# Kernel optimization log

Hardware: AMD Instinct MI355X
Metric: run time of the kernel (lower is better)

Reference implementation:

```python
import jax, jax.numpy as jnp
import numpy as np

B, S, H = 64, 2048, 256
H3 = 3 * H


def setup_inputs() -> dict:
    key = jax.random.key(0)
    ks = jax.random.split(key, 5)
    static = jax.random.normal(ks[0], (B, S, H), dtype=jnp.float32)
    dynamic = jax.random.normal(ks[1], (B, S, H), dtype=jnp.float32)
    decoder_hidden = jax.random.normal(ks[2], (B, H), dtype=jnp.float32)
    # learned params (nn.Parameter in original); scale ~ 1/sqrt(fan_in)
    v = jax.random.normal(ks[3], (1, H3), dtype=jnp.float32) / np.sqrt(H3)
    W = jax.random.normal(ks[4], (H3, H3), dtype=jnp.float32) / np.sqrt(H3)
    return {"static": static, "dynamic": dynamic,
            "decoder_hidden": decoder_hidden, "v": v, "W": W}


def reference(static, dynamic, decoder_hidden, v, W):
    # cat = concat(static[i,j], dynamic[i,j], decoder_hidden[i]) -> [B, S, 3H]
    dec = jnp.broadcast_to(decoder_hidden[:, None, :], static.shape)
    cat = jnp.concatenate([static, dynamic, dec], axis=-1)
    # score[b,s] = v . tanh(W @ cat[b,s])
    hidden = jnp.tanh(jnp.einsum('ok,bsk->bso', W, cat))  # [B, S, 3H]
    scores = jnp.einsum('bso,o->bs', hidden, v[0])        # [B, S]
    return jax.nn.softmax(scores, axis=1)
```

## Files before the change

### kernel.cpp

```cpp
#include <hip/hip_runtime.h>
#include <hip/hip_bf16.h>

#define B_   64
#define S_   2048
#define H_   256
#define H3_  768
#define K_   512
#define MT   64
#define RSTR 1040

typedef __attribute__((ext_vector_type(8))) short  bf16x8;
typedef __attribute__((ext_vector_type(4))) float  f32x4;

__device__ __forceinline__ uint pkbf2(float a, float b) {
    float2 f = make_float2(a, b);
    __hip_bfloat162 h = __float22bfloat162_rn(f);
    return *reinterpret_cast<uint*>(&h);
}

__global__ void pack_w(const float* __restrict__ W, short* __restrict__ wpk) {
    int t = blockIdx.x * 256 + threadIdx.x;
    if (t >= 48 * 16 * 64) return;
    int lane = t & 63;
    int ks   = (t >> 6) & 15;
    int ot   = t >> 10;
    int o  = ot * 16 + (lane & 15);
    int kb = ks * 32 + (lane >> 4) * 8;
    const float* src = W + (size_t)o * H3_ + kb;
    float4 a = ((const float4*)src)[0];
    float4 b = ((const float4*)src)[1];
    uint4 pk;
    pk.x = pkbf2(a.x, a.y);
    pk.y = pkbf2(a.z, a.w);
    pk.z = pkbf2(b.x, b.y);
    pk.w = pkbf2(b.z, b.w);
    *(uint4*)(wpk + (size_t)t * 8) = pk;
}

__global__ void bias_k(const float* __restrict__ W, const float* __restrict__ dec,
                       const float* __restrict__ v, float* __restrict__ bias,
                       float* __restrict__ vsum) {
    if (blockIdx.x == 192) {
        if (threadIdx.x < 64) {
            float s = 0.f;
#pragma unroll
            for (int i = 0; i < 12; ++i) s += v[threadIdx.x + i * 64];
#pragma unroll
            for (int off = 32; off >= 1; off >>= 1) s += __shfl_xor(s, off);
            if (threadIdx.x == 0) vsum[0] = s;
        }
        return;
    }
    int idx = blockIdx.x * 256 + threadIdx.x;
    int b = idx / H3_;
    int o = idx - b * H3_;
    const float4* wr = (const float4*)(W + (size_t)o * H3_ + 2 * H_);
    const float4* dv = (const float4*)(dec + (size_t)b * H_);
    float s = 0.f;
#pragma unroll 8
    for (int k = 0; k < H_ / 4; ++k) {
        float4 a = wr[k], d = dv[k];
        s += a.x * d.x + a.y * d.y + a.z * d.z + a.w * d.w;
    }
    bias[idx] = s;
}

__global__ __launch_bounds__(256, 2)
void score_k(const float* __restrict__ stat, const float* __restrict__ dyn,
             const short* __restrict__ wpk, const float* __restrict__ bias,
             const float* __restrict__ v, const float* __restrict__ vsum,
             float* __restrict__ scores) {
    __shared__ char  aT[MT * RSTR];
    __shared__ float sred[4][MT];

    const int tid  = threadIdx.x;
    const int pos0 = blockIdx.x * MT;
    const int bidx = pos0 >> 11;

#pragma unroll
    for (int bat = 0; bat < 2; ++bat) {
        float4 f0[8], f1[8];
#pragma unroll
        for (int u = 0; u < 8; ++u) {
            int lin = (bat * 8 + u) * 256 + tid;
            int row = lin >> 6;
            int k   = (lin & 63) * 8;
            const float* src = (k < 256)
                ? (stat + (size_t)(pos0 + row) * H_ + k)
                : (dyn  + (size_t)(pos0 + row) * H_ + (k - 256));
            f0[u] = ((const float4*)src)[0];
            f1[u] = ((const float4*)src)[1];
        }
#pragma unroll
        for (int u = 0; u < 8; ++u) {
            int lin = (bat * 8 + u) * 256 + tid;
            int row = lin >> 6;
            int ux  = lin & 63;
            uint4 pk;
            pk.x = pkbf2(f0[u].x, f0[u].y);
            pk.y = pkbf2(f0[u].z, f0[u].w);
            pk.z = pkbf2(f1[u].x, f1[u].y);
            pk.w = pkbf2(f1[u].z, f1[u].w);
            *(uint4*)(aT + row * RSTR + ux * 16) = pk;
        }
    }
    __syncthreads();

    const int wave = tid >> 6;
    const int lane = tid & 63;
    const int lr = lane & 15;
    const int lg = lane >> 4;

    const char* abase = aT + lr * RSTR + lg * 16;

    float sacc[4][4];
#pragma unroll
    for (int mi = 0; mi < 4; ++mi)
#pragma unroll
        for (int j = 0; j < 4; ++j) sacc[mi][j] = 0.f;

    const float C1 = 2.8853900817779268f;

#pragma unroll 1
    for (int pass = 0; pass < 3; ++pass) {
        const int obase = pass * 256 + wave * 64;

        float bv[4], vv2[4];
#pragma unroll
        for (int ni = 0; ni < 4; ++ni) {
            int o = obase + ni * 16 + lr;
            bv[ni]  = bias[bidx * H3_ + o];
            vv2[ni] = -2.0f * v[o];
        }

        f32x4 acc[4][4];
#pragma unroll
        for (int mi = 0; mi < 4; ++mi)
#pragma unroll
            for (int ni = 0; ni < 4; ++ni) {
                f32x4 a = {bv[ni], bv[ni], bv[ni], bv[ni]};
                acc[mi][ni] = a;
            }

        const short* wp0 = wpk + ((size_t)((pass * 16 + wave * 4) * 16) * 64 + lane) * 8;

#pragma unroll 4
        for (int ks = 0; ks < 16; ++ks) {
            bf16x8 bfr[4];
#pragma unroll
            for (int ni = 0; ni < 4; ++ni)
                bfr[ni] = *(const bf16x8*)(wp0 + ni * 16 * 64 * 8 + ks * 64 * 8);
            bf16x8 afr[4];
#pragma unroll
            for (int mi = 0; mi < 4; ++mi)
                afr[mi] = *(const bf16x8*)(abase + mi * 16 * RSTR + ks * 64);
#pragma unroll
            for (int mi = 0; mi < 4; ++mi)
#pragma unroll
                for (int ni = 0; ni < 4; ++ni)
                    acc[mi][ni] = __builtin_amdgcn_mfma_f32_16x16x32_bf16(
                        afr[mi], bfr[ni], acc[mi][ni], 0, 0, 0);
        }

#pragma unroll
        for (int ni = 0; ni < 4; ++ni)
#pragma unroll
            for (int mi = 0; mi < 4; ++mi)
#pragma unroll
                for (int j = 0; j < 4; ++j) {
                    float e = __builtin_amdgcn_exp2f(acc[mi][ni][j] * C1);
                    float r = __builtin_amdgcn_rcpf(e + 1.0f);
                    sacc[mi][j] = fmaf(vv2[ni], r, sacc[mi][j]);
                }
    }

#pragma unroll
    for (int mi = 0; mi < 4; ++mi)
#pragma unroll
        for (int j = 0; j < 4; ++j) {
            float x = sacc[mi][j];
            x += __shfl_xor(x, 1);
            x += __shfl_xor(x, 2);
            x += __shfl_xor(x, 4);
            x += __shfl_xor(x, 8);
            sacc[mi][j] = x;
        }
    if (lr == 0) {
#pragma unroll
        for (int mi = 0; mi < 4; ++mi)
#pragma unroll
            for (int j = 0; j < 4; ++j)
                sred[wave][mi * 16 + lg * 4 + j] = sacc[mi][j];
    }
    __syncthreads();
    if (tid < MT) {
        float s = vsum[0] + sred[0][tid] + sred[1][tid] + sred[2][tid] + sred[3][tid];
        scores[pos0 + tid] = s;
    }
}

__global__ void softmax_k(float* __restrict__ out) {
    const int b = blockIdx.x;
    float* row = out + (size_t)b * S_;
    const int tid  = threadIdx.x;
    const int wave = tid >> 6;
    const int lane = tid & 63;

    float vals[8];
    float m = -1e30f;
#pragma unroll
    for (int i = 0; i < 8; ++i) {
        vals[i] = row[tid + i * 256];
        m = fmaxf(m, vals[i]);
    }
#pragma unroll
    for (int off = 32; off >= 1; off >>= 1) m = fmaxf(m, __shfl_xor(m, off));
    __shared__ float redm[4];
    __shared__ float reds[4];
    if (lane == 0) redm[wave] = m;
    __syncthreads();
    m = fmaxf(fmaxf(redm[0], redm[1]), fmaxf(redm[2], redm[3]));

    float s = 0.f;
#pragma unroll
    for (int i = 0; i < 8; ++i) {
        vals[i] = __expf(vals[i] - m);
        s += vals[i];
    }
#pragma unroll
    for (int off = 32; off >= 1; off >>= 1) s += __shfl_xor(s, off);
    if (lane == 0) reds[wave] = s;
    __syncthreads();
    s = reds[0] + reds[1] + reds[2] + reds[3];
    float inv = 1.0f / s;
#pragma unroll
    for (int i = 0; i < 8; ++i) row[tid + i * 256] = vals[i] * inv;
}

extern "C" void kernel_launch(void* const* d_in, const int* in_sizes, int n_in,
                              void* d_out, int out_size, void* d_ws, size_t ws_size,
                              hipStream_t stream) {
    const float* stat = (const float*)d_in[0];
    const float* dyn  = (const float*)d_in[1];
    const float* dec  = (const float*)d_in[2];
    const float* v    = (const float*)d_in[3];
    const float* W    = (const float*)d_in[4];
    float* out = (float*)d_out;

    short* wpk  = (short*)d_ws;
    float* bias = (float*)((char*)d_ws + (size_t)H3_ * K_ * 2);
    float* vsum = bias + B_ * H3_;

    pack_w <<<(48 * 16 * 64 + 255) / 256, 256, 0, stream>>>(W, wpk);
    bias_k <<<193, 256, 0, stream>>>(W, dec, v, bias, vsum);
    score_k<<<(B_ * S_) / MT, 256, 0, stream>>>(stat, dyn, wpk, bias, v, vsum, out);
    softmax_k<<<B_, 256, 0, stream>>>(out);
}
```

Baseline: 147.7 us.

## Make score kernel persistent with double-buffered LDS prefetch across row tiles

The score kernel now launches 256 blocks of 512 threads. Each block processes 8 consecutive 64-row tiles, using double-buffered LDS. Global loads of the next tile's static and dynamic rows are interleaved between the MFMA phases of the current tile, so memory latency overlaps compute. Each of the 8 waves now owns 96 output columns, and bias and v are loaded once per block instead of per tile. This doubles LDS use and register pressure, and uses fewer, larger blocks, which may leave occupancy or load balance uneven.

```diff
diff --git a/kernel.cpp b/kernel.cpp
--- a/kernel.cpp
+++ b/kernel.cpp
@@ -7,7 +7,10 @@
 #define H3_  768
 #define K_   512
 #define MT   64
+#define TPB  8
+#define NB   256
 #define RSTR 1040
+#define BUFB (MT * RSTR)
 
 typedef __attribute__((ext_vector_type(8))) short  bf16x8;
 typedef __attribute__((ext_vector_type(4))) float  f32x4;
@@ -65,137 +68,214 @@
     bias[idx] = s;
 }
 
-__global__ __launch_bounds__(256, 2)
+__global__ __launch_bounds__(512, 2)
 void score_k(const float* __restrict__ stat, const float* __restrict__ dyn,
              const short* __restrict__ wpk, const float* __restrict__ bias,
              const float* __restrict__ v, const float* __restrict__ vsum,
              float* __restrict__ scores) {
-    __shared__ char  aT[MT * RSTR];
-    __shared__ float sred[4][MT];
+    __shared__ char  aT[2 * BUFB];
+    __shared__ float sred[2][8][MT];
 
     const int tid  = threadIdx.x;
-    const int pos0 = blockIdx.x * MT;
-    const int bidx = pos0 >> 11;
-
-#pragma unroll
-    for (int bat = 0; bat < 2; ++bat) {
-        float4 f0[8], f1[8];
-#pragma unroll
-        for (int u = 0; u < 8; ++u) {
-            int lin = (bat * 8 + u) * 256 + tid;
-            int row = lin >> 6;
-            int k   = (lin & 63) * 8;
-            const float* src = (k < 256)
-                ? (stat + (size_t)(pos0 + row) * H_ + k)
-                : (dyn  + (size_t)(pos0 + row) * H_ + (k - 256));
-            f0[u] = ((const float4*)src)[0];
-            f1[u] = ((const float4*)src)[1];
-        }
-#pragma unroll
-        for (int u = 0; u < 8; ++u) {
-            int lin = (bat * 8 + u) * 256 + tid;
-            int row = lin >> 6;
-            int ux  = lin & 63;
-            uint4 pk;
-            pk.x = pkbf2(f0[u].x, f0[u].y);
-            pk.y = pkbf2(f0[u].z, f0[u].w);
-            pk.z = pkbf2(f1[u].x, f1[u].y);
-            pk.w = pkbf2(f1[u].z, f1[u].w);
-            *(uint4*)(aT + row * RSTR + ux * 16) = pk;
-        }
-    }
-    __syncthreads();
-
     const int wave = tid >> 6;
     const int lane = tid & 63;
-    const int lr = lane & 15;
-    const int lg = lane >> 4;
-
-    const char* abase = aT + lr * RSTR + lg * 16;
-
-    float sacc[4][4];
-#pragma unroll
-    for (int mi = 0; mi < 4; ++mi)
-#pragma unroll
-        for (int j = 0; j < 4; ++j) sacc[mi][j] = 0.f;
-
+    const int lr   = lane & 15;
+    const int lg   = lane >> 4;
+
+    const int row0 = blockIdx.x * (TPB * MT);
+    const int bidx = row0 >> 11;
+
+    const float vs = vsum[0];
+
+    float bvA[2][3], vvA[2][3];
+#pragma unroll
+    for (int p = 0; p < 2; ++p)
+#pragma unroll
+        for (int ni = 0; ni < 3; ++ni) {
+            int o = wave * 96 + p * 48 + ni * 16 + lr;
+            bvA[p][ni] = bias[bidx * H3_ + o];
+            vvA[p][ni] = -2.0f * v[o];
+        }
+
+    const int kcol = lane * 8;
+    const float* srcbase = (kcol < 256) ? (stat + kcol) : (dyn + (kcol - 256));
+
+    float4 f0[3], f1[3];
+    auto loadu = [&](int u0, int n, int grow0) {
+#pragma unroll
+        for (int i = 0; i < n; ++i) {
+            int row = (u0 + i) * 8 + wave;
+            const float4* p = (const float4*)(srcbase + (size_t)(grow0 + row) * H_);
+            f0[i] = p[0];
+            f1[i] = p[1];
+        }
+    };
+    auto writeu = [&](int u0, int n, int bufoff) {
+#pragma unroll
+        for (int i = 0; i < n; ++i) {
+            int row = (u0 + i) * 8 + wave;
+            uint4 pk;
+            pk.x = pkbf2(f0[i].x, f0[i].y);
+            pk.y = pkbf2(f0[i].z, f0[i].w);
+            pk.z = pkbf2(f1[i].x, f1[i].y);
+            pk.w = pkbf2(f1[i].z, f1[i].w);
+            *(uint4*)(aT + bufoff + row * RSTR + lane * 16) = pk;
+        }
+    };
+
+    loadu(0, 3, row0); writeu(0, 3, 0);
+    loadu(3, 3, row0); writeu(3, 3, 0);
+    loadu(6, 2, row0); writeu(6, 2, 0);
+    __syncthreads();
+
+    const char* abase0 = aT + lr * RSTR + lg * 16;
     const float C1 = 2.8853900817779268f;
 
 #pragma unroll 1
-    for (int pass = 0; pass < 3; ++pass) {
-        const int obase = pass * 256 + wave * 64;
-
-        float bv[4], vv2[4];
-#pragma unroll
-        for (int ni = 0; ni < 4; ++ni) {
-            int o = obase + ni * 16 + lr;
-            bv[ni]  = bias[bidx * H3_ + o];
-            vv2[ni] = -2.0f * v[o];
-        }
-
-        f32x4 acc[4][4];
+    for (int t = 0; t < TPB; ++t) {
+        const int pos0 = row0 + t * MT;
+        const int cbuf = (t & 1) * BUFB;
+        const int nbuf = ((t & 1) ^ 1) * BUFB;
+        const int grown = pos0 + MT;
+        const bool pre = (t < TPB - 1);
+        const char* abase = abase0 + cbuf;
+
+        float sacc[4][4];
 #pragma unroll
         for (int mi = 0; mi < 4; ++mi)
 #pragma unroll
-            for (int ni = 0; ni < 4; ++ni) {
-                f32x4 a = {bv[ni], bv[ni], bv[ni], bv[ni]};
-                acc[mi][ni] = a;
+            for (int j = 0; j < 4; ++j) sacc[mi][j] = 0.f;
+
+        if (pre) loadu(0, 3, grown);
+
+        {
+            f32x4 acc[4][3];
+#pragma unroll
+            for (int mi = 0; mi < 4; ++mi)
+#pragma unroll
+                for (int ni = 0; ni < 3; ++ni) {
+                    f32x4 a = {bvA[0][ni], bvA[0][ni], bvA[0][ni], bvA[0][ni]};
+                    acc[mi][ni] = a;
+                }
+            const short* wp0 = wpk + (size_t)(wave * 6) * 8192 + lane * 8;
+#pragma unroll 4
+            for (int ks = 0; ks < 16; ++ks) {
+                bf16x8 bfr[3];
+#pragma unroll
+                for (int ni = 0; ni < 3; ++ni)
+                    bfr[ni] = *(const bf16x8*)(wp0 + ni * 8192 + ks * 512);
+                bf16x8 afr[4];
+#pragma unroll
+                for (int mi = 0; mi < 4; ++mi)
+                    afr[mi] = *(const bf16x8*)(abase + mi * (16 * RSTR) + ks * 64);
+#pragma unroll
+                for (int mi = 0; mi < 4; ++mi)
+#pragma unroll
+                    for (int ni = 0; ni < 3; ++ni)
+                        acc[mi][ni] = __builtin_amdgcn_mfma_f32_16x16x32_bf16(
+                            afr[mi], bfr[ni], acc[mi][ni], 0, 0, 0);
             }
-
-        const short* wp0 = wpk + ((size_t)((pass * 16 + wave * 4) * 16) * 64 + lane) * 8;
-
+#pragma unroll
+            for (int ni = 0; ni < 3; ++ni)
+#pragma unroll
+                for (int mi = 0; mi < 4; ++mi)
+#pragma unroll
+                    for (int j = 0; j < 4; ++j) {
+                        float e = __builtin_amdgcn_exp2f(acc[mi][ni][j] * C1);
+                        float r = __builtin_amdgcn_rcpf(e + 1.0f);
+                        sacc[mi][j] = fmaf(vvA[0][ni], r, sacc[mi][j]);
+                    }
+        }
+
+        if (pre) { writeu(0, 3, nbuf); loadu(3, 3, grown); }
+
+        {
+            f32x4 acc[4][3];
+#pragma unroll
+            for (int mi = 0; mi < 4; ++mi)
+#pragma unroll
+                for (int ni = 0; ni < 3; ++ni) {
+                    f32x4 a = {bvA[1][ni], bvA[1][ni], bvA[1][ni], bvA[1][ni]};
+                    acc[mi][ni] = a;
+                }
+            const short* wp1 = wpk + (size_t)(wave * 6 + 3) * 8192 + lane * 8;
 #pragma unroll 4
-        for (int ks = 0; ks < 16; ++ks) {
-            bf16x8 bfr[4];
-#pragma unroll
-            for (int ni = 0; ni < 4; ++ni)
-                bfr[ni] = *(const bf16x8*)(wp0 + ni * 16 * 64 * 8 + ks * 64 * 8);
-            bf16x8 afr[4];
+            for (int ks = 0; ks < 8; ++ks) {
+                bf16x8 bfr[3];
+#pragma unroll
+                for (int ni = 0; ni < 3; ++ni)
+                    bfr[ni] = *(const bf16x8*)(wp1 + ni * 8192 + ks * 512);
+                bf16x8 afr[4];
+#pragma unroll
+                for (int mi = 0; mi < 4; ++mi)
+                    afr[mi] = *(const bf16x8*)(abase + mi * (16 * RSTR) + ks * 64);
+#pragma unroll
+                for (int mi = 0; mi < 4; ++mi)
+#pragma unroll
+                    for (int ni = 0; ni < 3; ++ni)
+                        acc[mi][ni] = __builtin_amdgcn_mfma_f32_16x16x32_bf16(
+                            afr[mi], bfr[ni], acc[mi][ni], 0, 0, 0);
+            }
+
+            if (pre) { writeu(3, 3, nbuf); loadu(6, 2, grown); }
+
+#pragma unroll 4
+            for (int ks = 8; ks < 16; ++ks) {
+                bf16x8 bfr[3];
+#pragma unroll
+                for (int ni = 0; ni < 3; ++ni)
+                    bfr[ni] = *(const bf16x8*)(wp1 + ni * 8192 + ks * 512);
+                bf16x8 afr[4];
+#pragma unroll
+                for (int mi = 0; mi < 4; ++mi)
+                    afr[mi] = *(const bf16x8*)(abase + mi * (16 * RSTR) + ks * 64);
+#pragma unroll
+                for (int mi = 0; mi < 4; ++mi)
+#pragma unroll
+                    for (int ni = 0; ni < 3; ++ni)
+                        acc[mi][ni] = __builtin_amdgcn_mfma_f32_16x16x32_bf16(
+                            afr[mi], bfr[ni], acc[mi][ni], 0, 0, 0);
+            }
+
+            if (pre) writeu(6, 2, nbuf);
+
+#pragma unroll
+            for (int ni = 0; ni < 3; ++ni)
+#pragma unroll
+                for (int mi = 0; mi < 4; ++mi)
+#pragma unroll
+                    for (int j = 0; j < 4; ++j) {
+                        float e = __builtin_amdgcn_exp2f(acc[mi][ni][j] * C1);
+                        float r = __builtin_amdgcn_rcpf(e + 1.0f);
+                        sacc[mi][j] = fmaf(vvA[1][ni], r, sacc[mi][j]);
+                    }
+        }
+
+#pragma unroll
+        for (int mi = 0; mi < 4; ++mi)
+#pragma unroll
+            for (int j = 0; j < 4; ++j) {
+                float x = sacc[mi][j];
+                x += __shfl_xor(x, 1);
+                x += __shfl_xor(x, 2);
+                x += __shfl_xor(x, 4);
+                x += __shfl_xor(x, 8);
+                sacc[mi][j] = x;
+            }
+        if (lr == 0) {
 #pragma unroll
             for (int mi = 0; mi < 4; ++mi)
-                afr[mi] = *(const bf16x8*)(abase + mi * 16 * RSTR + ks * 64);
-#pragma unroll
-            for (int mi = 0; mi < 4; ++mi)
-#pragma unroll
-                for (int ni = 0; ni < 4; ++ni)
-                    acc[mi][ni] = __builtin_amdgcn_mfma_f32_16x16x32_bf16(
-                        afr[mi], bfr[ni], acc[mi][ni], 0, 0, 0);
-        }
-
-#pragma unroll
-        for (int ni = 0; ni < 4; ++ni)
-#pragma unroll
-            for (int mi = 0; mi < 4; ++mi)
-#pragma unroll
-                for (int j = 0; j < 4; ++j) {
-                    float e = __builtin_amdgcn_exp2f(acc[mi][ni][j] * C1);
-                    float r = __builtin_amdgcn_rcpf(e + 1.0f);
-                    sacc[mi][j] = fmaf(vv2[ni], r, sacc[mi][j]);
-                }
-    }
-
-#pragma unroll
-    for (int mi = 0; mi < 4; ++mi)
-#pragma unroll
-        for (int j = 0; j < 4; ++j) {
-            float x = sacc[mi][j];
-            x += __shfl_xor(x, 1);
-            x += __shfl_xor(x, 2);
-            x += __shfl_xor(x, 4);
-            x += __shfl_xor(x, 8);
-            sacc[mi][j] = x;
-        }
-    if (lr == 0) {
-#pragma unroll
-        for (int mi = 0; mi < 4; ++mi)
-#pragma unroll
-            for (int j = 0; j < 4; ++j)
-                sred[wave][mi * 16 + lg * 4 + j] = sacc[mi][j];
-    }
-    __syncthreads();
-    if (tid < MT) {
-        float s = vsum[0] + sred[0][tid] + sred[1][tid] + sred[2][tid] + sred[3][tid];
-        scores[pos0 + tid] = s;
+#pragma unroll
+                for (int j = 0; j < 4; ++j)
+                    sred[t & 1][wave][mi * 16 + lg * 4 + j] = sacc[mi][j];
+        }
+        __syncthreads();
+        if (tid < MT) {
+            float s = vs;
+#pragma unroll
+            for (int w = 0; w < 8; ++w) s += sred[t & 1][w][tid];
+            scores[pos0 + tid] = s;
+        }
     }
 }
 
@@ -253,6 +333,6 @@
 
     pack_w <<<(48 * 16 * 64 + 255) / 256, 256, 0, stream>>>(W, wpk);
     bias_k <<<193, 256, 0, stream>>>(W, dec, v, bias, vsum);
-    score_k<<<(B_ * S_) / MT, 256, 0, stream>>>(stat, dyn, wpk, bias, v, vsum, out);
+    score_k<<<NB, 512, 0, stream>>>(stat, dyn, wpk, bias, v, vsum, out);
     softmax_k<<<B_, 256, 0, stream>>>(out);
 }
```

Measured after the change: 154.6 us. 1.05x slower.
